# Kernel tuning notes

Measured on AMD Instinct MI355X. Metric: run time of the kernel, lower is better.

Reference implementation:

```python
import jax, jax.numpy as jnp
import numpy as np

B, S, H = 2, 2048, 1024
E, K, F = 8, 2, 4096


def setup_inputs() -> dict:
    key = jax.random.key(0)
    ks = jax.random.split(key, 7)
    s_h = 1.0 / np.sqrt(H)
    s_f = 1.0 / np.sqrt(F)
    return {
        "hidden_states": jax.random.normal(ks[0], (B, S, H), jnp.float32),
        "Wr": jax.random.normal(ks[1], (H, E), jnp.float32) * s_h,
        "br": jnp.zeros((E,), jnp.float32),
        "W1": jax.random.normal(ks[2], (E, H, F), jnp.float32) * s_h,
        "b1": jnp.zeros((E, F), jnp.float32),
        "W2": jax.random.normal(ks[3], (E, F, H), jnp.float32) * s_f,
        "b2": jnp.zeros((E, H), jnp.float32),
    }


def _moe_forward(hidden_states, Wr, br, W1, b1, W2, b2):
    b, s, h = hidden_states.shape
    x = hidden_states.reshape(-1, h)  # [T, H]
    # --- router: top-k over softmax probs, renormalized ---
    logits = x @ Wr + br  # [T, E]
    probs = jax.nn.softmax(logits, axis=-1)
    top_w, top_i = jax.lax.top_k(probs, K)  # [T, K]
    weights = top_w / jnp.sum(top_w, axis=-1, keepdims=True)  # [T, K]
    # --- dense-equivalent expert dispatch + combine ---
    # per-token per-expert combine weight (zero for unselected experts)
    out = jnp.zeros_like(x)
    for e in range(E):
        w_e = jnp.sum(weights * (top_i == e), axis=-1)  # [T]
        h_e = jax.nn.gelu(x @ W1[e] + b1[e], approximate=False)  # [T, F]
        y_e = h_e @ W2[e] + b2[e]  # [T, H]
        out = out + w_e[:, None] * y_e
    # --- aux load-balance loss (counts are constants wrt grads) ---
    counts = jnp.sum(jax.nn.one_hot(top_i, E, dtype=logits.dtype), axis=(0, 1))  # [E]
    load = counts / (top_i.size)
    aux_loss = jnp.mean((load - 1.0 / E) ** 2)
    # --- z-loss ---
    z_loss = jnp.mean(jax.nn.logsumexp(logits, axis=-1))
    total_loss = 0.01 * aux_loss + 0.001 * z_loss
    return out.reshape(b, s, h), total_loss


def reference(hidden_states, Wr, br, W1, b1, W2, b2):
    output, total_loss = _moe_forward(hidden_states, Wr, br, W1, b1, W2, b2)
    return output, total_loss
```

## Files before the change

### kernel.cpp

```cpp
#include <hip/hip_runtime.h>
#include <stdint.h>
#include <math.h>

#define T_TOK 4096
#define H_DIM 1024
#define E_EXP 8
#define F_DIM 4096
#define NASSIGN (T_TOK * 2)
#define OUT_ELEMS ((size_t)T_TOK * H_DIM)
#define YB_ELEMS ((size_t)8192 * H_DIM)

typedef unsigned short u16;
typedef __attribute__((ext_vector_type(8))) short short8;
typedef __attribute__((ext_vector_type(4))) float f32x4;

__device__ __forceinline__ u16 f2bf(float f) {
  union { float f; uint32_t u; } c; c.f = f;
  uint32_t u = c.u;
  return (u16)((u + 0x7FFFu + ((u >> 16) & 1u)) >> 16);
}

__device__ __forceinline__ void gl_lds16(const void* g, void* l) {
  __builtin_amdgcn_global_load_lds(
      (const __attribute__((address_space(1))) uint32_t*)g,
      (__attribute__((address_space(3))) uint32_t*)(uintptr_t)l, 16, 0, 0);
}

__global__ __launch_bounds__(256) void transpose_cvt_tiled(
    const float* __restrict__ in, u16* __restrict__ out, int R, int C) {
  __shared__ u16 tile[64][72];
  const size_t eoff = (size_t)blockIdx.z * R * C;
  {
    const int c4 = (threadIdx.x & 15) * 4;
    const int rr = threadIdx.x >> 4;
    const float* inp = in + eoff + ((size_t)blockIdx.y * 64) * C + blockIdx.x * 64;
#pragma unroll
    for (int p = 0; p < 4; ++p) {
      const int r = rr + p * 16;
      const float4 v = *(const float4*)(inp + (size_t)r * C + c4);
      tile[r][c4 + 0] = f2bf(v.x); tile[r][c4 + 1] = f2bf(v.y);
      tile[r][c4 + 2] = f2bf(v.z); tile[r][c4 + 3] = f2bf(v.w);
    }
  }
  __syncthreads();
  {
    u16* op = out + (((size_t)blockIdx.z * (C >> 6) + blockIdx.x) * (R >> 6)
                     + blockIdx.y) * 4096;
#pragma unroll
    for (int p = 0; p < 2; ++p) {
      const int c = (threadIdx.x >> 3) + p * 32;
      const int rg = (threadIdx.x & 7) * 8;
      short8 o;
#pragma unroll
      for (int j = 0; j < 8; ++j) o[j] = (short)tile[rg + j][c];
      *(short8*)(op + c * 64 + rg) = o;
    }
  }
}

__global__ void router_kernel(const float* __restrict__ x, const float* __restrict__ Wr,
                              const float* __restrict__ br, u16* __restrict__ xb,
                              int* __restrict__ tki, float* __restrict__ tkw,
                              int* __restrict__ counts, float* __restrict__ zsum) {
  const int wave = threadIdx.x >> 6;
  const int lane = threadIdx.x & 63;
  __shared__ int lcnt[8];
  __shared__ float lzv[16];
  if (threadIdx.x < 8) lcnt[threadIdx.x] = 0;
  __syncthreads();
#pragma unroll
  for (int it = 0; it < 4; ++it) {
    const int t = blockIdx.x * 16 + wave * 4 + it;
    const float* xr = x + (size_t)t * H_DIM;
    u16* xbr = xb + (size_t)t * H_DIM;
    float acc[8];
#pragma unroll
    for (int e = 0; e < 8; ++e) acc[e] = 0.0f;
#pragma unroll
    for (int j = 0; j < 16; ++j) {
      const int hh = j * 64 + lane;
      const float xv = xr[hh];
      xbr[hh] = f2bf(xv);
      const float4 w0 = *(const float4*)(Wr + (size_t)hh * 8);
      const float4 w1 = *(const float4*)(Wr + (size_t)hh * 8 + 4);
      acc[0] += xv * w0.x; acc[1] += xv * w0.y; acc[2] += xv * w0.z; acc[3] += xv * w0.w;
      acc[4] += xv * w1.x; acc[5] += xv * w1.y; acc[6] += xv * w1.z; acc[7] += xv * w1.w;
    }
#pragma unroll
    for (int e = 0; e < 8; ++e) {
      float v = acc[e];
#pragma unroll
      for (int s = 32; s > 0; s >>= 1) v += __shfl_xor(v, s);
      acc[e] = v;
    }
    if (lane == 0) {
      float l[8];
#pragma unroll
      for (int e = 0; e < 8; ++e) l[e] = acc[e] + br[e];
      float mx = l[0];
#pragma unroll
      for (int e = 1; e < 8; ++e) mx = fmaxf(mx, l[e]);
      float p[8], s = 0.0f;
#pragma unroll
      for (int e = 0; e < 8; ++e) { p[e] = __expf(l[e] - mx); s += p[e]; }
      int i0 = 0;
#pragma unroll
      for (int e = 1; e < 8; ++e) if (p[e] > p[i0]) i0 = e;
      int i1 = (i0 == 0) ? 1 : 0;
#pragma unroll
      for (int e = 0; e < 8; ++e) if (e != i1 && e != i0 && p[e] > p[i1]) i1 = e;
      const float ws = p[i0] + p[i1];
      tki[2 * t] = i0; tki[2 * t + 1] = i1;
      tkw[2 * t] = p[i0] / ws; tkw[2 * t + 1] = p[i1] / ws;
      atomicAdd(&lcnt[i0], 1);
      atomicAdd(&lcnt[i1], 1);
      lzv[wave * 4 + it] = mx + logf(s);
    }
  }
  __syncthreads();
  if (threadIdx.x < 8) {
    const int c = lcnt[threadIdx.x];
    if (c) atomicAdd(&counts[threadIdx.x], c);
  }
  if (threadIdx.x == 64) {
    float zs = 0.0f;
#pragma unroll
    for (int i = 0; i < 16; ++i) zs += lzv[i];
    atomicAdd(zsum, zs);
  }
}

__global__ void scatter_kernel(const int* __restrict__ tki, const float* __restrict__ tkw,
                               const int* __restrict__ counts, int* __restrict__ cursor,
                               int* __restrict__ perm, float* __restrict__ pw,
                               int* __restrict__ islot,
                               const float* __restrict__ zsum, float* __restrict__ out_loss) {
  int offs[8];
  {
    int a = 0;
#pragma unroll
    for (int e = 0; e < 8; ++e) { offs[e] = a; a += counts[e]; }
  }
  const int lane = threadIdx.x & 63;
  const int t = blockIdx.x * 256 + threadIdx.x;
#pragma unroll
  for (int k = 0; k < 2; ++k) {
    const int e = tki[2 * t + k];
    int slot = 0;
#pragma unroll
    for (int ee = 0; ee < 8; ++ee) {
      const unsigned long long mask = __ballot(e == ee);
      if (mask) {
        const int leader = __ffsll(mask) - 1;
        int b = 0;
        if (lane == leader) b = atomicAdd(&cursor[ee], (int)__popcll(mask));
        b = __shfl(b, leader);
        if (e == ee) {
          const int r = (int)__popcll(mask & ((1ull << lane) - 1ull));
          slot = offs[ee] + b + r;
        }
      }
    }
    perm[slot] = t;
    pw[slot] = tkw[2 * t + k];
    islot[2 * t + k] = slot;
  }
  if (blockIdx.x == 0 && threadIdx.x == 0) {
    float aux = 0.0f;
#pragma unroll
    for (int e = 0; e < 8; ++e) {
      const float d = (float)counts[e] / (float)NASSIGN - 0.125f;
      aux += d * d;
    }
    aux *= (1.0f / 8.0f);
    out_loss[0] = 0.01f * aux + 0.001f * (zsum[0] / (float)T_TOK);
  }
}


__global__ __launch_bounds__(256, 4) void gemm1_kernel(
    const u16* __restrict__ xb, const u16* __restrict__ w1t,
    const float* __restrict__ b1, const int* __restrict__ perm,
    const int* __restrict__ cnts, u16* __restrict__ hbuf) {
  const int id = blockIdx.x;
  const int e = id & 7;
  const int wq = id >> 3;
  const int n0 = (wq & 31) << 7;
  const int m0 = (wq >> 5) << 7;
  int cnt, off;
  {
    int a = 0, c = 0;
#pragma unroll
    for (int i = 0; i < 8; ++i) { const int ci = cnts[i]; if (i < e) a += ci; if (i == e) c = ci; }
    cnt = c; off = a;
  }
  if (m0 >= cnt) return;

  __shared__ __align__(16) u16 smem[16384];
  u16* As = smem;
  u16* Bs = smem + 8192;

  const int tid = threadIdx.x;
  const int rbase = tid >> 3;
  const int kc = ((tid & 7) ^ (rbase & 7)) * 8;

  const u16* ap[4];
#pragma unroll
  for (int l = 0; l < 4; ++l) {
    int ra = m0 + rbase + l * 32; if (ra > cnt - 1) ra = cnt - 1;
    ap[l] = xb + (size_t)perm[off + ra] * H_DIM + kc;
  }
  const u16* bp0 = w1t + ((((size_t)e * (F_DIM >> 6) + (n0 >> 6)) * (H_DIM >> 6)) << 12)
                 + rbase * 64 + kc;
  const size_t bnt = (size_t)(H_DIM >> 6) << 12;

  const int wave = tid >> 6, lane = tid & 63;
  const int wm = (wave >> 1) * 64, wn = (wave & 1) * 64;
  const int lr = lane & 15, q = lane >> 4;
  const int qs0 = q ^ (lr & 7), qs1 = (4 + q) ^ (lr & 7);

  f32x4 acc[4][4];
#pragma unroll
  for (int i = 0; i < 4; ++i)
#pragma unroll
    for (int j = 0; j < 4; ++j) acc[i][j] = (f32x4)0.0f;

  const short8* Afr = (const short8*)As;
  const short8* Bfr = (const short8*)Bs;

  for (int k0 = 0; k0 < (H_DIM >> 6); ++k0) {
    gl_lds16(ap[0], &As[(size_t)tid * 8]);
    gl_lds16(ap[1], &As[(size_t)(tid + 256) * 8]);
    gl_lds16(ap[2], &As[(size_t)(tid + 512) * 8]);
    gl_lds16(ap[3], &As[(size_t)(tid + 768) * 8]);
    gl_lds16(bp0,              &Bs[(size_t)tid * 8]);
    gl_lds16(bp0 + 2048,       &Bs[(size_t)(tid + 256) * 8]);
    gl_lds16(bp0 + bnt,        &Bs[(size_t)(tid + 512) * 8]);
    gl_lds16(bp0 + bnt + 2048, &Bs[(size_t)(tid + 768) * 8]);
#pragma unroll
    for (int l = 0; l < 4; ++l) ap[l] += 64;
    bp0 += 4096;
    __syncthreads();
#pragma unroll
    for (int s = 0; s < 2; ++s) {
      const int qs = s ? qs1 : qs0;
      short8 a[4], b[4];
#pragma unroll
      for (int i = 0; i < 4; ++i) a[i] = Afr[(wm + i * 16 + lr) * 8 + qs];
#pragma unroll
      for (int j = 0; j < 4; ++j) b[j] = Bfr[(wn + j * 16 + lr) * 8 + qs];
#pragma unroll
      for (int i = 0; i < 4; ++i)
#pragma unroll
        for (int j = 0; j < 4; ++j)
          acc[i][j] = __builtin_amdgcn_mfma_f32_16x16x32_bf16(a[i], b[j], acc[i][j], 0, 0, 0);
    }
    __syncthreads();
  }

#pragma unroll
  for (int i = 0; i < 4; ++i) {
#pragma unroll
    for (int rr = 0; rr < 4; ++rr) {
      const int row = wm + i * 16 + q * 4 + rr;
#pragma unroll
      for (int j = 0; j < 4; ++j) {
        const int col = wn + j * 16 + lr;
        const float v = acc[i][j][rr] + b1[e * F_DIM + n0 + col];
        const float g = 0.5f * v * (1.0f + erff(v * 0.70710678118654752f));
        smem[(row << 7) + (col ^ (q << 4))] = f2bf(g);
      }
    }
  }
  __syncthreads();
#pragma unroll
  for (int p = 0; p < 8; ++p) {
    const int ml = p * 16 + (tid >> 4);
    const int nl = (tid & 15) * 8;
    const int m = m0 + ml;
    if (m < cnt) {
      const int qq = (ml >> 2) & 3;
      *(short8*)(hbuf + (size_t)(off + m) * F_DIM + n0 + nl) =
          *(const short8*)(smem + (ml << 7) + (nl ^ (qq << 4)));
    }
  }
}

__global__ __launch_bounds__(256, 4) void gemm2_kernel(
    const u16* __restrict__ hbuf, const u16* __restrict__ w2t,
    const float* __restrict__ b2, const float* __restrict__ pw,
    const int* __restrict__ cnts, float* __restrict__ ybuf) {
  const int id = blockIdx.x;
  const int e = id & 7;
  const int wq = id >> 3;
  const int n0 = (wq & 7) << 7;
  const int ks = (wq >> 3) & 1;
  const int m0 = (wq >> 4) << 7;
  int cnt, off;
  {
    int a = 0, c = 0;
#pragma unroll
    for (int i = 0; i < 8; ++i) { const int ci = cnts[i]; if (i < e) a += ci; if (i == e) c = ci; }
    cnt = c; off = a;
  }
  if (m0 >= cnt) return;

  __shared__ __align__(16) u16 As[128 * 64];
  __shared__ __align__(16) u16 Bs[128 * 64];

  const int tid = threadIdx.x;
  const int rbase = tid >> 3;
  const int kc = ((tid & 7) ^ (rbase & 7)) * 8;

  const u16* ap[4];
#pragma unroll
  for (int l = 0; l < 4; ++l) {
    int ra = m0 + rbase + l * 32; if (ra > cnt - 1) ra = cnt - 1;
    ap[l] = hbuf + (size_t)(off + ra) * F_DIM + (ks << 11) + kc;
  }
  const u16* bp0 = w2t + ((((size_t)e * (H_DIM >> 6) + (n0 >> 6)) * (F_DIM >> 6)) << 12)
                 + ((size_t)(ks << 5) << 12) + rbase * 64 + kc;
  const size_t bnt = (size_t)(F_DIM >> 6) << 12;

  const int wave = tid >> 6, lane = tid & 63;
  const int wm = (wave >> 1) * 64, wn = (wave & 1) * 64;
  const int lr = lane & 15, q = lane >> 4;
  const int qs0 = q ^ (lr & 7), qs1 = (4 + q) ^ (lr & 7);

  f32x4 acc[4][4];
#pragma unroll
  for (int i = 0; i < 4; ++i)
#pragma unroll
    for (int j = 0; j < 4; ++j) acc[i][j] = (f32x4)0.0f;

  const short8* Afr = (const short8*)As;
  const short8* Bfr = (const short8*)Bs;

  for (int k0 = 0; k0 < 32; ++k0) {
    gl_lds16(ap[0], &As[(size_t)tid * 8]);
    gl_lds16(ap[1], &As[(size_t)(tid + 256) * 8]);
    gl_lds16(ap[2], &As[(size_t)(tid + 512) * 8]);
    gl_lds16(ap[3], &As[(size_t)(tid + 768) * 8]);
    gl_lds16(bp0,              &Bs[(size_t)tid * 8]);
    gl_lds16(bp0 + 2048,       &Bs[(size_t)(tid + 256) * 8]);
    gl_lds16(bp0 + bnt,        &Bs[(size_t)(tid + 512) * 8]);
    gl_lds16(bp0 + bnt + 2048, &Bs[(size_t)(tid + 768) * 8]);
#pragma unroll
    for (int l = 0; l < 4; ++l) ap[l] += 64;
    bp0 += 4096;
    __syncthreads();
#pragma unroll
    for (int s = 0; s < 2; ++s) {
      const int qs = s ? qs1 : qs0;
      short8 a[4], b[4];
#pragma unroll
      for (int i = 0; i < 4; ++i) a[i] = Afr[(wm + i * 16 + lr) * 8 + qs];
#pragma unroll
      for (int j = 0; j < 4; ++j) b[j] = Bfr[(wn + j * 16 + lr) * 8 + qs];
#pragma unroll
      for (int i = 0; i < 4; ++i)
#pragma unroll
        for (int j = 0; j < 4; ++j)
          acc[i][j] = __builtin_amdgcn_mfma_f32_16x16x32_bf16(a[i], b[j], acc[i][j], 0, 0, 0);
    }
    __syncthreads();
  }

  float* yb = ybuf + (size_t)ks * YB_ELEMS;
#pragma unroll
  for (int i = 0; i < 4; ++i) {
#pragma unroll
    for (int rr = 0; rr < 4; ++rr) {
      const int m = m0 + wm + i * 16 + q * 4 + rr;
      if (m < cnt) {
        const int slot = off + m;
        const float w = pw[slot];
        float* orow = yb + (size_t)slot * H_DIM;
#pragma unroll
        for (int j = 0; j < 4; ++j) {
          const int col = n0 + wn + j * 16 + lr;
          float y = acc[i][j][rr];
          if (ks == 0) y += b2[e * H_DIM + col];
          orow[col] = w * y;
        }
      }
    }
  }
}

__global__ __launch_bounds__(256) void combine_kernel(
    const float* __restrict__ ybuf, const int* __restrict__ islot,
    float* __restrict__ out) {
  const int t = blockIdx.x;
  const int s0 = islot[2 * t];
  const int s1 = islot[2 * t + 1];
  const int c = threadIdx.x * 4;
  const float4 a0 = *(const float4*)(ybuf + (size_t)s0 * H_DIM + c);
  const float4 a1 = *(const float4*)(ybuf + YB_ELEMS + (size_t)s0 * H_DIM + c);
  const float4 b0 = *(const float4*)(ybuf + (size_t)s1 * H_DIM + c);
  const float4 b1 = *(const float4*)(ybuf + YB_ELEMS + (size_t)s1 * H_DIM + c);
  float4 r;
  r.x = a0.x + a1.x + b0.x + b1.x;
  r.y = a0.y + a1.y + b0.y + b1.y;
  r.z = a0.z + a1.z + b0.z + b1.z;
  r.w = a0.w + a1.w + b0.w + b1.w;
  *(float4*)(out + (size_t)t * H_DIM + c) = r;
}


extern "C" void kernel_launch(void* const* d_in, const int* in_sizes, int n_in,
                              void* d_out, int out_size, void* d_ws, size_t ws_size,
                              hipStream_t stream) {
  const float* x  = (const float*)d_in[0];
  const float* Wr = (const float*)d_in[1];
  const float* br = (const float*)d_in[2];
  const float* W1 = (const float*)d_in[3];
  const float* b1 = (const float*)d_in[4];
  const float* W2 = (const float*)d_in[5];
  const float* b2 = (const float*)d_in[6];
  float* out = (float*)d_out;

  char* ws = (char*)d_ws;
  u16* xb    = (u16*)(ws);
  u16* w1t   = (u16*)(ws + 8388608ull);
  u16* w2t   = (u16*)(ws + 75497472ull);
  u16* hbuf  = (u16*)(ws + 142606336ull);
  float* ybuf = (float*)(ws + 8388608ull);
  int*   tki    = (int*)(ws + 209715200ull);
  float* tkw    = (float*)(ws + 209747968ull);
  int*   perm   = (int*)(ws + 209780736ull);
  float* pw     = (float*)(ws + 209813504ull);
  int*   counts = (int*)(ws + 209846272ull);
  int*   cursor = counts + 8;
  float* zsum   = (float*)(counts + 16);
  int*   islot  = (int*)(ws + 209846400ull);

  hipMemsetAsync(counts, 0, 128, stream);

  transpose_cvt_tiled<<<dim3(F_DIM / 64, H_DIM / 64, E_EXP), 256, 0, stream>>>(W1, w1t, H_DIM, F_DIM);
  transpose_cvt_tiled<<<dim3(H_DIM / 64, F_DIM / 64, E_EXP), 256, 0, stream>>>(W2, w2t, F_DIM, H_DIM);
  router_kernel<<<T_TOK / 16, 256, 0, stream>>>(x, Wr, br, xb, tki, tkw, counts, zsum);
  scatter_kernel<<<T_TOK / 256, 256, 0, stream>>>(tki, tkw, counts, cursor, perm, pw,
                                                  islot, zsum, out + OUT_ELEMS);
  gemm1_kernel<<<8192, 256, 0, stream>>>(xb, w1t, b1, perm, counts, hbuf);
  gemm2_kernel<<<4096, 256, 0, stream>>>(hbuf, w2t, b2, pw, counts, ybuf);
  combine_kernel<<<T_TOK, 256, 0, stream>>>(ybuf, islot, out);
}
```

Baseline: 608.1 us.

## Enlarge expert GEMM tiles to 256x256 with 512 threads and double-buffered LDS

Both expert GEMMs move from 128x128 tiles with 256 threads to 256x256 tiles with 512 threads (8 waves, each computing 128x64). LDS grows to 128 KB and is split into two buffers, so the next K-slice loads while the current one is consumed and one barrier per iteration is dropped. The aim is more reuse per loaded byte and overlap of global-to-LDS traffic with MFMA work. In exchange each thread needs more registers, residency drops to one block per CU, and padding waste grows for experts whose token count is not a multiple of 256.

```diff
diff --git a/kernel.cpp b/kernel.cpp
--- a/kernel.cpp
+++ b/kernel.cpp
@@ -178,15 +178,15 @@
 }
 
 
-__global__ __launch_bounds__(256, 4) void gemm1_kernel(
+__global__ __launch_bounds__(512, 2) void gemm1_kernel(
     const u16* __restrict__ xb, const u16* __restrict__ w1t,
     const float* __restrict__ b1, const int* __restrict__ perm,
     const int* __restrict__ cnts, u16* __restrict__ hbuf) {
   const int id = blockIdx.x;
   const int e = id & 7;
   const int wq = id >> 3;
-  const int n0 = (wq & 31) << 7;
-  const int m0 = (wq >> 5) << 7;
+  const int n0 = (wq & 15) << 8;
+  const int m0 = (wq >> 4) << 8;
   int cnt, off;
   {
     int a = 0, c = 0;
@@ -196,9 +196,7 @@
   }
   if (m0 >= cnt) return;
 
-  __shared__ __align__(16) u16 smem[16384];
-  u16* As = smem;
-  u16* Bs = smem + 8192;
+  __shared__ __align__(16) u16 smem[65536];
 
   const int tid = threadIdx.x;
   const int rbase = tid >> 3;
@@ -207,59 +205,65 @@
   const u16* ap[4];
 #pragma unroll
   for (int l = 0; l < 4; ++l) {
-    int ra = m0 + rbase + l * 32; if (ra > cnt - 1) ra = cnt - 1;
+    int ra = m0 + rbase + l * 64; if (ra > cnt - 1) ra = cnt - 1;
     ap[l] = xb + (size_t)perm[off + ra] * H_DIM + kc;
   }
-  const u16* bp0 = w1t + ((((size_t)e * (F_DIM >> 6) + (n0 >> 6)) * (H_DIM >> 6)) << 12)
-                 + rbase * 64 + kc;
-  const size_t bnt = (size_t)(H_DIM >> 6) << 12;
+  const u16* bp[4];
+#pragma unroll
+  for (int l = 0; l < 4; ++l)
+    bp[l] = w1t + (((size_t)e * (F_DIM >> 6) + (n0 >> 6) + l) * (H_DIM >> 6)) * 4096
+          + rbase * 64 + kc;
 
   const int wave = tid >> 6, lane = tid & 63;
-  const int wm = (wave >> 1) * 64, wn = (wave & 1) * 64;
+  const int wm = (wave >> 2) * 128, wn = (wave & 3) * 64;
   const int lr = lane & 15, q = lane >> 4;
   const int qs0 = q ^ (lr & 7), qs1 = (4 + q) ^ (lr & 7);
 
-  f32x4 acc[4][4];
-#pragma unroll
-  for (int i = 0; i < 4; ++i)
+  f32x4 acc[8][4];
+#pragma unroll
+  for (int i = 0; i < 8; ++i)
 #pragma unroll
     for (int j = 0; j < 4; ++j) acc[i][j] = (f32x4)0.0f;
 
-  const short8* Afr = (const short8*)As;
-  const short8* Bfr = (const short8*)Bs;
+  int cur = 0;
+#pragma unroll
+  for (int l = 0; l < 4; ++l) {
+    gl_lds16(ap[l], &smem[tid * 8 + l * 4096]);           ap[l] += 64;
+    gl_lds16(bp[l], &smem[16384 + tid * 8 + l * 4096]);   bp[l] += 4096;
+  }
+  __syncthreads();
 
   for (int k0 = 0; k0 < (H_DIM >> 6); ++k0) {
-    gl_lds16(ap[0], &As[(size_t)tid * 8]);
-    gl_lds16(ap[1], &As[(size_t)(tid + 256) * 8]);
-    gl_lds16(ap[2], &As[(size_t)(tid + 512) * 8]);
-    gl_lds16(ap[3], &As[(size_t)(tid + 768) * 8]);
-    gl_lds16(bp0,              &Bs[(size_t)tid * 8]);
-    gl_lds16(bp0 + 2048,       &Bs[(size_t)(tid + 256) * 8]);
-    gl_lds16(bp0 + bnt,        &Bs[(size_t)(tid + 512) * 8]);
-    gl_lds16(bp0 + bnt + 2048, &Bs[(size_t)(tid + 768) * 8]);
-#pragma unroll
-    for (int l = 0; l < 4; ++l) ap[l] += 64;
-    bp0 += 4096;
-    __syncthreads();
+    if (k0 + 1 < (H_DIM >> 6)) {
+      const int nb = (cur ^ 1) << 15;
+#pragma unroll
+      for (int l = 0; l < 4; ++l) {
+        gl_lds16(ap[l], &smem[nb + tid * 8 + l * 4096]);           ap[l] += 64;
+        gl_lds16(bp[l], &smem[nb + 16384 + tid * 8 + l * 4096]);   bp[l] += 4096;
+      }
+    }
+    const short8* Af = (const short8*)(smem + (cur << 15));
+    const short8* Bf = Af + 2048;
 #pragma unroll
     for (int s = 0; s < 2; ++s) {
       const int qs = s ? qs1 : qs0;
-      short8 a[4], b[4];
-#pragma unroll
-      for (int i = 0; i < 4; ++i) a[i] = Afr[(wm + i * 16 + lr) * 8 + qs];
-#pragma unroll
-      for (int j = 0; j < 4; ++j) b[j] = Bfr[(wn + j * 16 + lr) * 8 + qs];
-#pragma unroll
-      for (int i = 0; i < 4; ++i)
+      short8 a[8], b[4];
+#pragma unroll
+      for (int i = 0; i < 8; ++i) a[i] = Af[(wm + i * 16 + lr) * 8 + qs];
+#pragma unroll
+      for (int j = 0; j < 4; ++j) b[j] = Bf[(wn + j * 16 + lr) * 8 + qs];
+#pragma unroll
+      for (int i = 0; i < 8; ++i)
 #pragma unroll
         for (int j = 0; j < 4; ++j)
           acc[i][j] = __builtin_amdgcn_mfma_f32_16x16x32_bf16(a[i], b[j], acc[i][j], 0, 0, 0);
     }
     __syncthreads();
-  }
-
-#pragma unroll
-  for (int i = 0; i < 4; ++i) {
+    cur ^= 1;
+  }
+
+#pragma unroll
+  for (int i = 0; i < 8; ++i) {
 #pragma unroll
     for (int rr = 0; rr < 4; ++rr) {
       const int row = wm + i * 16 + q * 4 + rr;
@@ -268,34 +272,34 @@
         const int col = wn + j * 16 + lr;
         const float v = acc[i][j][rr] + b1[e * F_DIM + n0 + col];
         const float g = 0.5f * v * (1.0f + erff(v * 0.70710678118654752f));
-        smem[(row << 7) + (col ^ (q << 4))] = f2bf(g);
+        smem[(row << 8) + (col ^ (q << 4))] = f2bf(g);
       }
     }
   }
   __syncthreads();
 #pragma unroll
-  for (int p = 0; p < 8; ++p) {
-    const int ml = p * 16 + (tid >> 4);
-    const int nl = (tid & 15) * 8;
-    const int m = m0 + ml;
+  for (int p = 0; p < 16; ++p) {
+    const int row = p * 16 + (tid >> 5);
+    const int nl = (tid & 31) * 8;
+    const int m = m0 + row;
     if (m < cnt) {
-      const int qq = (ml >> 2) & 3;
+      const int qq = (row >> 2) & 3;
       *(short8*)(hbuf + (size_t)(off + m) * F_DIM + n0 + nl) =
-          *(const short8*)(smem + (ml << 7) + (nl ^ (qq << 4)));
-    }
-  }
-}
-
-__global__ __launch_bounds__(256, 4) void gemm2_kernel(
+          *(const short8*)(smem + (row << 8) + (nl ^ (qq << 4)));
+    }
+  }
+}
+
+__global__ __launch_bounds__(512, 2) void gemm2_kernel(
     const u16* __restrict__ hbuf, const u16* __restrict__ w2t,
     const float* __restrict__ b2, const float* __restrict__ pw,
     const int* __restrict__ cnts, float* __restrict__ ybuf) {
   const int id = blockIdx.x;
   const int e = id & 7;
   const int wq = id >> 3;
-  const int n0 = (wq & 7) << 7;
-  const int ks = (wq >> 3) & 1;
-  const int m0 = (wq >> 4) << 7;
+  const int n0 = (wq & 3) << 8;
+  const int ks = (wq >> 2) & 1;
+  const int m0 = (wq >> 3) << 8;
   int cnt, off;
   {
     int a = 0, c = 0;
@@ -305,8 +309,7 @@
   }
   if (m0 >= cnt) return;
 
-  __shared__ __align__(16) u16 As[128 * 64];
-  __shared__ __align__(16) u16 Bs[128 * 64];
+  __shared__ __align__(16) u16 smem[65536];
 
   const int tid = threadIdx.x;
   const int rbase = tid >> 3;
@@ -315,60 +318,66 @@
   const u16* ap[4];
 #pragma unroll
   for (int l = 0; l < 4; ++l) {
-    int ra = m0 + rbase + l * 32; if (ra > cnt - 1) ra = cnt - 1;
+    int ra = m0 + rbase + l * 64; if (ra > cnt - 1) ra = cnt - 1;
     ap[l] = hbuf + (size_t)(off + ra) * F_DIM + (ks << 11) + kc;
   }
-  const u16* bp0 = w2t + ((((size_t)e * (H_DIM >> 6) + (n0 >> 6)) * (F_DIM >> 6)) << 12)
-                 + ((size_t)(ks << 5) << 12) + rbase * 64 + kc;
-  const size_t bnt = (size_t)(F_DIM >> 6) << 12;
+  const u16* bp[4];
+#pragma unroll
+  for (int l = 0; l < 4; ++l)
+    bp[l] = w2t + (((size_t)e * (H_DIM >> 6) + (n0 >> 6) + l) * (F_DIM >> 6)
+                   + (ks << 5)) * 4096 + rbase * 64 + kc;
 
   const int wave = tid >> 6, lane = tid & 63;
-  const int wm = (wave >> 1) * 64, wn = (wave & 1) * 64;
+  const int wm = (wave >> 2) * 128, wn = (wave & 3) * 64;
   const int lr = lane & 15, q = lane >> 4;
   const int qs0 = q ^ (lr & 7), qs1 = (4 + q) ^ (lr & 7);
 
-  f32x4 acc[4][4];
-#pragma unroll
-  for (int i = 0; i < 4; ++i)
+  f32x4 acc[8][4];
+#pragma unroll
+  for (int i = 0; i < 8; ++i)
 #pragma unroll
     for (int j = 0; j < 4; ++j) acc[i][j] = (f32x4)0.0f;
 
-  const short8* Afr = (const short8*)As;
-  const short8* Bfr = (const short8*)Bs;
+  int cur = 0;
+#pragma unroll
+  for (int l = 0; l < 4; ++l) {
+    gl_lds16(ap[l], &smem[tid * 8 + l * 4096]);           ap[l] += 64;
+    gl_lds16(bp[l], &smem[16384 + tid * 8 + l * 4096]);   bp[l] += 4096;
+  }
+  __syncthreads();
 
   for (int k0 = 0; k0 < 32; ++k0) {
-    gl_lds16(ap[0], &As[(size_t)tid * 8]);
-    gl_lds16(ap[1], &As[(size_t)(tid + 256) * 8]);
-    gl_lds16(ap[2], &As[(size_t)(tid + 512) * 8]);
-    gl_lds16(ap[3], &As[(size_t)(tid + 768) * 8]);
-    gl_lds16(bp0,              &Bs[(size_t)tid * 8]);
-    gl_lds16(bp0 + 2048,       &Bs[(size_t)(tid + 256) * 8]);
-    gl_lds16(bp0 + bnt,        &Bs[(size_t)(tid + 512) * 8]);
-    gl_lds16(bp0 + bnt + 2048, &Bs[(size_t)(tid + 768) * 8]);
-#pragma unroll
-    for (int l = 0; l < 4; ++l) ap[l] += 64;
-    bp0 += 4096;
-    __syncthreads();
+    if (k0 + 1 < 32) {
+      const int nb = (cur ^ 1) << 15;
+#pragma unroll
+      for (int l = 0; l < 4; ++l) {
+        gl_lds16(ap[l], &smem[nb + tid * 8 + l * 4096]);           ap[l] += 64;
+        gl_lds16(bp[l], &smem[nb + 16384 + tid * 8 + l * 4096]);   bp[l] += 4096;
+      }
+    }
+    const short8* Af = (const short8*)(smem + (cur << 15));
+    const short8* Bf = Af + 2048;
 #pragma unroll
     for (int s = 0; s < 2; ++s) {
       const int qs = s ? qs1 : qs0;
-      short8 a[4], b[4];
-#pragma unroll
-      for (int i = 0; i < 4; ++i) a[i] = Afr[(wm + i * 16 + lr) * 8 + qs];
-#pragma unroll
-      for (int j = 0; j < 4; ++j) b[j] = Bfr[(wn + j * 16 + lr) * 8 + qs];
-#pragma unroll
-      for (int i = 0; i < 4; ++i)
+      short8 a[8], b[4];
+#pragma unroll
+      for (int i = 0; i < 8; ++i) a[i] = Af[(wm + i * 16 + lr) * 8 + qs];
+#pragma unroll
+      for (int j = 0; j < 4; ++j) b[j] = Bf[(wn + j * 16 + lr) * 8 + qs];
+#pragma unroll
+      for (int i = 0; i < 8; ++i)
 #pragma unroll
         for (int j = 0; j < 4; ++j)
           acc[i][j] = __builtin_amdgcn_mfma_f32_16x16x32_bf16(a[i], b[j], acc[i][j], 0, 0, 0);
     }
     __syncthreads();
+    cur ^= 1;
   }
 
   float* yb = ybuf + (size_t)ks * YB_ELEMS;
 #pragma unroll
-  for (int i = 0; i < 4; ++i) {
+  for (int i = 0; i < 8; ++i) {
 #pragma unroll
     for (int rr = 0; rr < 4; ++rr) {
       const int m = m0 + wm + i * 16 + q * 4 + rr;
@@ -442,7 +451,7 @@
   router_kernel<<<T_TOK / 16, 256, 0, stream>>>(x, Wr, br, xb, tki, tkw, counts, zsum);
   scatter_kernel<<<T_TOK / 256, 256, 0, stream>>>(tki, tkw, counts, cursor, perm, pw,
                                                   islot, zsum, out + OUT_ELEMS);
-  gemm1_kernel<<<8192, 256, 0, stream>>>(xb, w1t, b1, perm, counts, hbuf);
-  gemm2_kernel<<<4096, 256, 0, stream>>>(hbuf, w2t, b2, pw, counts, ybuf);
+  gemm1_kernel<<<2048, 512, 0, stream>>>(xb, w1t, b1, perm, counts, hbuf);
+  gemm2_kernel<<<1024, 512, 0, stream>>>(hbuf, w2t, b2, pw, counts, ybuf);
   combine_kernel<<<T_TOK, 256, 0, stream>>>(ybuf, islot, out);
 }
```

Result: slower. 620.8 us (+2.1%).
